# Kernel tuning notes

Hardware: AMD Instinct MI355X
Metric: run time of the kernel (lower is better)

The kernel has to match this reference:

```python
import jax, jax.numpy as jnp
import numpy as np

NH = 12  # num_heads


def setup_inputs() -> dict:
    key = jax.random.key(0)
    k1, k2, k3 = jax.random.split(key, 3)
    B, Hs, Ws, C = 8, 56, 56, 768
    N = Hs * Ws + 1  # +1 cls token
    x = jax.random.normal(k1, (B, N, C), jnp.float32)
    W_qkv = jax.random.normal(k2, (C, 3 * C), jnp.float32) * 0.02  # qkv_bias=False
    W_proj = jax.random.normal(k3, (C, C), jnp.float32) * 0.02
    b_proj = jnp.zeros((C,), jnp.float32)
    return {"x": x, "W_qkv": W_qkv, "W_proj": W_proj, "b_proj": b_proj}


def _criss_cross(x, W_qkv, W_proj, b_proj):
    B, N, C = x.shape
    H = W = int(np.sqrt(N))  # N = H*W + 1 (cls token); int(sqrt(3137)) == 56
    hd = C // NH
    scale = hd ** -0.5
    qkv = (x @ W_qkv).reshape(B, N, 3, NH, hd).transpose(2, 0, 3, 1, 4)
    q, k, v = qkv[0], qkv[1], qkv[2]  # (B, NH, N, hd)
    q_cls, k_cls, v_cls = q[:, :, :1], k[:, :, :1], v[:, :, :1]  # (B, NH, 1, hd)

    def grid(t):  # drop cls, view as spatial grid (B, NH, H, W, hd)
        return t[:, :, 1:].reshape(B, NH, H, W, hd)

    def col_view(t, t_cls):  # column (height) axis with cls prepended: (B, W, NH, 1+H, hd)
        tg = jnp.transpose(grid(t), (0, 3, 1, 2, 4))
        cls = jnp.broadcast_to(t_cls[:, None], (B, W, NH, 1, hd))
        return jnp.concatenate([cls, tg], axis=3)

    def row_view(t):  # row (width) axis: (B, H, NH, W, hd)
        return jnp.transpose(grid(t), (0, 2, 1, 3, 4))

    q_h, k_h, v_h = col_view(q, q_cls), col_view(k, k_cls), col_view(v, v_cls)
    q_w, k_w, v_w = row_view(q), row_view(k), row_view(v)

    s_h = jnp.einsum('bwnqd,bwnkd->bwnqk', q_h, k_h) * scale  # (B, W, NH, 1+H, 1+H)
    s_h = jnp.transpose(s_h, (0, 3, 2, 1, 4))[:, 1:]          # (B, H, NH, W, 1+H)
    s_w = jnp.einsum('bhnqd,bhnkd->bhnqk', q_w, k_w) * scale  # (B, H, NH, W, W)
    s_w = jnp.where(jnp.eye(W, dtype=bool), -jnp.inf, s_w)    # mask self in row attention

    # joint softmax over concatenated column+row scores
    attn = jax.nn.softmax(jnp.concatenate([s_h, s_w], axis=-1), axis=-1)
    a_h, a_w = attn[..., :1 + H], attn[..., 1 + H:]
    a_h = jnp.transpose(a_h, (0, 3, 2, 1, 4))  # (B, W, NH, H, 1+H)

    x_h = jnp.einsum('bwnqk,bwnkd->bqwnd', a_h, v_h).reshape(B, H, W, C)
    x_w = jnp.einsum('bhnqk,bhnkd->bhqnd', a_w, v_w).reshape(B, H, W, C)
    out = (x_h + x_w).reshape(B, H * W, C)

    # cls token attends over the full sequence (including itself)
    s_cls = jnp.einsum('bnqd,bnkd->bnqk', q_cls, k) * scale  # (B, NH, 1, N)
    a_cls = jax.nn.softmax(s_cls, axis=-1)
    x_cls = jnp.einsum('bnqk,bnkd->bqnd', a_cls, v).reshape(B, 1, C)

    out = jnp.concatenate([x_cls, out], axis=1)  # (B, N, C)
    return out @ W_proj + b_proj


def reference(x, W_qkv, W_proj, b_proj):
    return _criss_cross(x, W_qkv, W_proj, b_proj)
```

## Files before the change

### kernel.cpp

```cpp
#include <hip/hip_runtime.h>
#include <math.h>

#define B_   8
#define Hs   56
#define Ws   56
#define Cc   768
#define NHh  12
#define HDd  64
#define Nt   3137
#define HW_  3136
#define C3   2304
#define SCALE 0.125f
#define Mrows (B_ * Nt)
#define Mpad  (99 * 256)

typedef _Float16 half8  __attribute__((ext_vector_type(8)));
typedef _Float16 half4  __attribute__((ext_vector_type(4)));
typedef _Float16 half2_ __attribute__((ext_vector_type(2)));
typedef float floatx4 __attribute__((ext_vector_type(4)));

#define WAITV(N) asm volatile("s_waitcnt vmcnt(" #N ")" ::: "memory")
#define WAITL    asm volatile("s_waitcnt lgkmcnt(0)" ::: "memory")

__device__ __forceinline__ void barrier_mem() {
    asm volatile("" ::: "memory");
    __builtin_amdgcn_s_barrier();
    asm volatile("" ::: "memory");
}

__device__ __forceinline__ void gload_lds16(const _Float16* g, _Float16* l) {
    __builtin_amdgcn_global_load_lds(
        (const __attribute__((address_space(1))) void*)g,
        (__attribute__((address_space(3))) void*)l, 16, 0, 0);
}

__device__ _Float16 g_qkvh[(size_t)Mrows * C3];
__device__ float    g_Ocol[(size_t)B_ * NHh * HW_ * HDd];
__device__ float    g_mcol[(size_t)B_ * NHh * HW_];
__device__ float    g_lcol[(size_t)B_ * NHh * HW_];
__device__ _Float16 g_xh[(size_t)Mpad * Cc];
__device__ _Float16 g_attH[(size_t)Mpad * Cc];
__device__ _Float16 g_WqkvT[(size_t)C3 * Cc];
__device__ _Float16 g_WprojT[(size_t)Cc * Cc];
__device__ float    g_clsP[(size_t)B_ * NHh * 4 * 66];

__global__ __launch_bounds__(256) void cvt_f16(
    const float* __restrict__ in, _Float16* __restrict__ out, int n4)
{
    for (int i = blockIdx.x * 256 + threadIdx.x; i < n4; i += gridDim.x * 256) {
        float4 v = ((const float4*)in)[i];
        half4 h = { (_Float16)v.x, (_Float16)v.y, (_Float16)v.z, (_Float16)v.w };
        ((half4*)out)[i] = h;
    }
}

__global__ __launch_bounds__(256) void transpose_f16(
    const float* __restrict__ in, _Float16* __restrict__ out, int R, int Cq)
{
    __shared__ float t[32][33];
    const int c0 = blockIdx.x * 32, r0 = blockIdx.y * 32;
    const int tx = threadIdx.x & 31, ty = threadIdx.x >> 5;
#pragma unroll
    for (int i = 0; i < 32; i += 8)
        t[ty + i][tx] = in[(size_t)(r0 + ty + i) * Cq + c0 + tx];
    __syncthreads();
#pragma unroll
    for (int i = 0; i < 32; i += 8)
        out[(size_t)(c0 + ty + i) * R + r0 + tx] = (_Float16)t[tx][ty + i];
}

template <typename OutT, int BM>
__global__ __launch_bounds__(512, 2) void gemm_f16(
    const _Float16* __restrict__ A, const _Float16* __restrict__ Bt,
    const float* __restrict__ bias, OutT* __restrict__ Cm,
    int M, int Nd, int K)
{
    constexpr int MI   = BM / 32;
    constexpr int MIH  = MI / 2;
    constexpr int LA   = BM / 128;
    constexpr int ASZh = BM * 64;
    constexpr int BSZh = 256 * 64;
    constexpr size_t MAINB = (size_t)2 * (ASZh + BSZh) * 2;
    constexpr size_t EPIB  = sizeof(OutT) == 2 ? (size_t)BM * 280 * 2
                                               : (size_t)BM * 140 * 4;
    constexpr size_t SMEMB = MAINB > EPIB ? MAINB : EPIB;
    __shared__ __align__(16) char smem[SMEMB];

    const int tid = threadIdx.x;
    const int wave = tid >> 6, lane = tid & 63;
    const int wm = wave & 1, wn = wave >> 1;

    const int bid = blockIdx.y * gridDim.x + blockIdx.x;
    const int perPanel = gridDim.x * 16;
    const int panel = bid / perPanel;
    const int rowsIn = min(16, (int)gridDim.y - panel * 16);
    const int rem = bid - panel * perPanel;
    const int by = panel * 16 + rem % rowsIn;
    const int bx = rem / rowsIn;
    const int mBase = by * BM, nBase = bx * 256;

    const int rU  = ((tid >> 7) << 4) + (tid & 15);
    const int kcU = (tid >> 4) & 7;

    auto stageHalf = [&](int kt, int h) {
        _Float16* arena = (_Float16*)smem + (size_t)(kt & 1) * (ASZh + BSZh);
        if (h < 2) {
            _Float16* ldsA = arena + h * (ASZh / 2) + tid * 8;
            const _Float16* g = A + (size_t)(mBase + h * (BM / 2) + rU) * K
                                  + kt * 64 + kcU * 8;
#pragma unroll
            for (int j = 0; j < LA; ++j)
                gload_lds16(g + (size_t)j * 64 * K, ldsA + j * 4096);
        } else {
            const int hh = h - 2;
            _Float16* ldsB = arena + ASZh + hh * (BSZh / 2) + tid * 8;
            const _Float16* g = Bt + (size_t)(nBase + hh * 128 + rU) * K
                                   + kt * 64 + kcU * 8;
#pragma unroll
            for (int j = 0; j < 2; ++j)
                gload_lds16(g + (size_t)j * 64 * K, ldsB + j * 4096);
        }
    };

    const int fo = (lane >> 4) * 128 + (lane & 15) * 8;

    floatx4 acc[MI][4] = {};
    half8 a[MIH], b[4];

    const int NT = K >> 6;
    stageHalf(0, 0); stageHalf(0, 1); stageHalf(0, 2); stageHalf(0, 3);

    for (int t = 0; t < NT; ++t) {
        const _Float16* aA = (const _Float16*)smem
                             + (size_t)(t & 1) * (ASZh + BSZh);
        const _Float16* aB = aA + ASZh;
        const bool st = (t + 1 < NT);

        if (st) stageHalf(t + 1, 0);
        if (!st) { WAITV(0); }
        else if constexpr (LA == 2) { WAITV(2); }
        else { WAITV(1); }
        barrier_mem();
#pragma unroll
        for (int ni = 0; ni < 4; ++ni)
            b[ni] = *(const half8*)&aB[(wn * 4 + ni) * 1024 + fo];
#pragma unroll
        for (int mi = 0; mi < MIH; ++mi)
            a[mi] = *(const half8*)&aA[(wm * MI + mi) * 1024 + fo];
        WAITL;
        __builtin_amdgcn_s_setprio(1);
#pragma unroll
        for (int mi = 0; mi < MIH; ++mi)
#pragma unroll
            for (int ni = 0; ni < 4; ++ni)
                acc[mi][ni] = __builtin_amdgcn_mfma_f32_16x16x32_f16(
                    b[ni], a[mi], acc[mi][ni], 0, 0, 0);
        __builtin_amdgcn_s_setprio(0);
        barrier_mem();

        if (st) stageHalf(t + 1, 1);
#pragma unroll
        for (int mi = 0; mi < MIH; ++mi)
            a[mi] = *(const half8*)&aA[(wm * MI + MIH + mi) * 1024 + fo];
        WAITL;
        __builtin_amdgcn_s_setprio(1);
#pragma unroll
        for (int mi = 0; mi < MIH; ++mi)
#pragma unroll
            for (int ni = 0; ni < 4; ++ni)
                acc[MIH + mi][ni] = __builtin_amdgcn_mfma_f32_16x16x32_f16(
                    b[ni], a[mi], acc[MIH + mi][ni], 0, 0, 0);
        __builtin_amdgcn_s_setprio(0);
        barrier_mem();

        if (st) stageHalf(t + 1, 2);
#pragma unroll
        for (int ni = 0; ni < 4; ++ni)
            b[ni] = *(const half8*)&aB[(wn * 4 + ni) * 1024 + 512 + fo];
#pragma unroll
        for (int mi = 0; mi < MIH; ++mi)
            a[mi] = *(const half8*)&aA[(wm * MI + mi) * 1024 + 512 + fo];
        WAITL;
        __builtin_amdgcn_s_setprio(1);
#pragma unroll
        for (int mi = 0; mi < MIH; ++mi)
#pragma unroll
            for (int ni = 0; ni < 4; ++ni)
                acc[mi][ni] = __builtin_amdgcn_mfma_f32_16x16x32_f16(
                    b[ni], a[mi], acc[mi][ni], 0, 0, 0);
        __builtin_amdgcn_s_setprio(0);
        barrier_mem();

        if (st) stageHalf(t + 1, 3);
#pragma unroll
        for (int mi = 0; mi < MIH; ++mi)
            a[mi] = *(const half8*)&aA[(wm * MI + MIH + mi) * 1024 + 512 + fo];
        WAITL;
        __builtin_amdgcn_s_setprio(1);
#pragma unroll
        for (int mi = 0; mi < MIH; ++mi)
#pragma unroll
            for (int ni = 0; ni < 4; ++ni)
                acc[MIH + mi][ni] = __builtin_amdgcn_mfma_f32_16x16x32_f16(
                    b[ni], a[mi], acc[MIH + mi][ni], 0, 0, 0);
        __builtin_amdgcn_s_setprio(0);
        barrier_mem();
    }

    const int mlBase = wm * (BM / 2) + (lane & 15);
    const int nlBase = wn * 64 + ((lane >> 4) << 2);

    if constexpr (sizeof(OutT) == 2) {
        _Float16* Ch = (_Float16*)smem;
#pragma unroll
        for (int ni = 0; ni < 4; ++ni) {
            const int nl = nlBase + ni * 16;
#pragma unroll
            for (int mi = 0; mi < MI; ++mi) {
                const int ml = mlBase + mi * 16;
                floatx4 v = acc[mi][ni];
                half4 h = { (_Float16)v[0], (_Float16)v[1],
                            (_Float16)v[2], (_Float16)v[3] };
                *(half4*)&Ch[ml * 280 + nl] = h;
            }
        }
        barrier_mem();
#pragma unroll
        for (int i = 0; i < BM / 16; ++i) {
            const int f = i * 512 + tid;
            const int row = f >> 5, u = f & 31;
            const int gm = mBase + row;
            if (gm < M)
                *(half8*)&Cm[(size_t)gm * Nd + nBase + u * 8] =
                    *(const half8*)&Ch[row * 280 + u * 8];
        }
    } else {
        float* Cf = (float*)smem;
#pragma unroll
        for (int nh = 0; nh < 2; ++nh) {
            barrier_mem();
            if ((wn >> 1) == nh) {
#pragma unroll
                for (int ni = 0; ni < 4; ++ni) {
                    const int n0 = nBase + wn * 64 + ((lane >> 4) << 2) + ni * 16;
                    float4 bv = bias ? *(const float4*)&bias[n0]
                                     : make_float4(0.f, 0.f, 0.f, 0.f);
                    const int nl = (wn & 1) * 64 + ((lane >> 4) << 2) + ni * 16;
#pragma unroll
                    for (int mi = 0; mi < MI; ++mi) {
                        const int ml = mlBase + mi * 16;
                        floatx4 v = acc[mi][ni];
                        float4 o = make_float4(v[0] + bv.x, v[1] + bv.y,
                                               v[2] + bv.z, v[3] + bv.w);
                        *(float4*)&Cf[ml * 140 + nl] = o;
                    }
                }
            }
            barrier_mem();
#pragma unroll
            for (int i = 0; i < BM / 16; ++i) {
                const int f = i * 512 + tid;
                const int row = f >> 5, u = f & 31;
                const int gm = mBase + row;
                if (gm < M)
                    *(float4*)&Cm[(size_t)gm * Nd + nBase + nh * 128 + u * 4] =
                        *(const float4*)&Cf[row * 140 + u * 4];
            }
        }
    }
}

template <int MODE>
__global__ __launch_bounds__(64) void cc_attn(
    const _Float16* __restrict__ qkvh,
    float* __restrict__ Ocol, float* __restrict__ mcol,
    float* __restrict__ lcol, _Float16* __restrict__ attH)
{
    constexpr int NK = (MODE == 0) ? 57 : 56;
    const int x = blockIdx.x, nh = blockIdx.y, b = blockIdx.z;
    const int lane = threadIdx.x;
    const int q15 = lane & 15, g = lane >> 4;

    __shared__ __align__(16) char smem[18944];
    _Float16* Vt = (_Float16*)smem;
    _Float16* Pl = (_Float16*)(smem + 9216);
    float*    ML = (float*)(smem + 18432);
    float*    Ol = (float*)smem;

    const _Float16* base_b = qkvh + (size_t)(b * Nt) * C3 + nh * HDd;

    auto nrow_k = [&](int key) -> int {
        key = min(key, NK - 1);
        if (MODE == 0) return (key == 0) ? 0 : ((key - 1) * Ws + x + 1);
        return x * Ws + key + 1;
    };
    auto nrow_q = [&](int q) -> int {
        q = min(q, 55);
        return (MODE == 0) ? (q * Ws + x + 1) : (x * Ws + q + 1);
    };

    half8 Kf[4][2], Qf[4][2];
#pragma unroll
    for (int t = 0; t < 4; ++t) {
        const _Float16* kp = base_b + (size_t)nrow_k(t * 16 + q15) * C3 + Cc;
        const _Float16* qp = base_b + (size_t)nrow_q(t * 16 + q15) * C3;
#pragma unroll
        for (int kk = 0; kk < 2; ++kk) {
            Kf[t][kk] = *(const half8*)(kp + kk * 32 + g * 8);
            Qf[t][kk] = *(const half8*)(qp + kk * 32 + g * 8);
        }
    }

#pragma unroll
    for (int it = 0; it < 8; ++it) {
        const int i = it * 64 + lane;
        const int j = i >> 3, c = i & 7;
        half8 v = {};
        if (j < NK)
            v = *(const half8*)(base_b + (size_t)nrow_k(j) * C3 + 2 * Cc + c * 8);
#pragma unroll
        for (int e = 0; e < 8; ++e)
            Vt[(c * 8 + e) * 72 + ((j + 8 * c) & 63)] = v[e];
    }

    floatx4 S[4][4] = {};
#pragma unroll
    for (int kt = 0; kt < 4; ++kt)
#pragma unroll
        for (int qt = 0; qt < 4; ++qt)
#pragma unroll
            for (int kk = 0; kk < 2; ++kk)
                S[kt][qt] = __builtin_amdgcn_mfma_f32_16x16x32_f16(
                    Kf[kt][kk], Qf[qt][kk], S[kt][qt], 0, 0, 0);

    float mq[4], lq[4];
#pragma unroll
    for (int qt = 0; qt < 4; ++qt) {
        const int q = qt * 16 + q15;
        float sv[4][4];
        float mm = -1e30f;
#pragma unroll
        for (int kt = 0; kt < 4; ++kt)
#pragma unroll
            for (int r = 0; r < 4; ++r) {
                const int key = kt * 16 + g * 4 + r;
                float s = S[kt][qt][r] * SCALE;
                const bool bad = (key >= NK) || (MODE == 1 && key == q);
                sv[kt][r] = bad ? -1e30f : s;
                mm = fmaxf(mm, sv[kt][r]);
            }
        mm = fmaxf(mm, __shfl_xor(mm, 16, 64));
        mm = fmaxf(mm, __shfl_xor(mm, 32, 64));
        float ll = 0.f;
#pragma unroll
        for (int kt = 0; kt < 4; ++kt) {
            half4 ph;
#pragma unroll
            for (int r = 0; r < 4; ++r) {
                const float p = __expf(sv[kt][r] - mm);
                ll += p;
                ph[r] = (_Float16)p;
            }
            *(half4*)&Pl[q * 72 + kt * 16 + g * 4] = ph;
        }
        ll += __shfl_xor(ll, 16, 64);
        ll += __shfl_xor(ll, 32, 64);
        mq[qt] = mm; lq[qt] = ll;
    }

    if (g == 0) {
        if (MODE == 0) {
#pragma unroll
            for (int qt = 0; qt < 4; ++qt) {
                const int q = qt * 16 + q15;
                if (q < 56) {
                    const size_t qi = (size_t)((b * NHh + nh) * HW_) + q * Ws + x;
                    mcol[qi] = mq[qt]; lcol[qi] = lq[qt];
                }
            }
        } else {
#pragma unroll
            for (int qt = 0; qt < 4; ++qt) {
                ML[qt * 16 + q15] = mq[qt];
                ML[64 + qt * 16 + q15] = lq[qt];
            }
        }
    }
    __syncthreads();

    half8 Pf[4][2];
#pragma unroll
    for (int qt = 0; qt < 4; ++qt)
#pragma unroll
        for (int kk = 0; kk < 2; ++kk)
            Pf[qt][kk] = *(const half8*)&Pl[(qt * 16 + q15) * 72 + kk * 32 + g * 8];

    floatx4 O[4][4] = {};
#pragma unroll
    for (int dt = 0; dt < 4; ++dt) {
        const int d = dt * 16 + q15;
        const int rot = 8 * (d >> 3);
        half8 Vf0 = *(const half8*)&Vt[d * 72 + ((0 + g * 8 + rot) & 63)];
        half8 Vf1 = *(const half8*)&Vt[d * 72 + ((32 + g * 8 + rot) & 63)];
#pragma unroll
        for (int qt = 0; qt < 4; ++qt) {
            O[dt][qt] = __builtin_amdgcn_mfma_f32_16x16x32_f16(
                Vf0, Pf[qt][0], O[dt][qt], 0, 0, 0);
            O[dt][qt] = __builtin_amdgcn_mfma_f32_16x16x32_f16(
                Vf1, Pf[qt][1], O[dt][qt], 0, 0, 0);
        }
    }
    __syncthreads();

#pragma unroll
    for (int dt = 0; dt < 4; ++dt)
#pragma unroll
        for (int qt = 0; qt < 4; ++qt) {
            float4 f = { O[dt][qt][0], O[dt][qt][1], O[dt][qt][2], O[dt][qt][3] };
            *(float4*)&Ol[(qt * 16 + q15) * 68 + dt * 16 + g * 4] = f;
        }
    __syncthreads();

    const int qq = lane;
    if (qq < 56) {
        if (MODE == 0) {
            const size_t qi = (size_t)((b * NHh + nh) * HW_) + qq * Ws + x;
            float* op = Ocol + qi * HDd;
#pragma unroll
            for (int i = 0; i < 16; ++i)
                *(float4*)(op + i * 4) = *(const float4*)&Ol[qq * 68 + i * 4];
        } else {
            const size_t qi = (size_t)((b * NHh + nh) * HW_) + x * Ws + qq;
            const float mc = mcol[qi], lc = lcol[qi];
            const float mr = ML[qq], lr = ML[64 + qq];
            const float mn = fmaxf(mc, mr);
            const float fc = __expf(mc - mn);
            const float fr = __expf(mr - mn);
            const float inv = 1.f / (lc * fc + lr * fr);
            const int n = x * Ws + qq + 1;
            _Float16* op = attH + (size_t)(b * Nt + n) * Cc + nh * HDd;
            const float* ocp = Ocol + qi * HDd;
#pragma unroll
            for (int i = 0; i < 16; ++i) {
                float4 oc = *(const float4*)(ocp + i * 4);
                const float* oo = &Ol[qq * 68 + i * 4];
                half4 r = { (_Float16)((oc.x * fc + oo[0] * fr) * inv),
                            (_Float16)((oc.y * fc + oo[1] * fr) * inv),
                            (_Float16)((oc.z * fc + oo[2] * fr) * inv),
                            (_Float16)((oc.w * fc + oo[3] * fr) * inv) };
                *(half4*)(op + i * 4) = r;
            }
        }
    }
}

__global__ __launch_bounds__(1024) void cls_part(
    const _Float16* __restrict__ qkvh, float* __restrict__ P)
{
    const int nh = blockIdx.x, b = blockIdx.y, sidx = blockIdx.z;
    const int j0 = sidx * 785, j1 = min(Nt, j0 + 785);
    const int tid = threadIdx.x;
    const int lane = tid & 63, wv = tid >> 6;

    const float qd = (float)qkvh[(size_t)(b * Nt) * C3 + nh * HDd + lane];
    float m = -INFINITY, l = 0.f, Od = 0.f;

    for (int j = j0 + wv; j < j1; j += 16) {
        const _Float16* base = qkvh + (size_t)(b * Nt + j) * C3 + nh * HDd;
        float prod = qd * (float)base[Cc + lane];
#pragma unroll
        for (int off = 32; off >= 1; off >>= 1)
            prod += __shfl_xor(prod, off, 64);
        float s = prod * SCALE;
        float mn = fmaxf(m, s);
        float corr = __expf(m - mn);
        float p = __expf(s - mn);
        l = l * corr + p;
        Od = fmaf(Od, corr, p * (float)base[2 * Cc + lane]);
        m = mn;
    }

    __shared__ float sm[16], sl[16], sO[16][64];
    if (lane == 0) { sm[wv] = m; sl[wv] = l; }
    sO[wv][lane] = Od;
    __syncthreads();

    if (tid < 64) {
        float M2 = sm[0];
#pragma unroll
        for (int i = 1; i < 16; ++i) M2 = fmaxf(M2, sm[i]);
        float L = 0.f, OO = 0.f;
#pragma unroll
        for (int i = 0; i < 16; ++i) {
            float f = __expf(sm[i] - M2);
            L += sl[i] * f;
            OO += sO[i][tid] * f;
        }
        float* pp = P + (size_t)((b * NHh + nh) * 4 + sidx) * 66;
        if (tid == 0) { pp[0] = M2; pp[1] = L; }
        pp[2 + tid] = OO;
    }
}

__global__ __launch_bounds__(64) void cls_merge(
    const float* __restrict__ P, _Float16* __restrict__ attH)
{
    const int nh = blockIdx.x, b = blockIdx.y;
    const int tid = threadIdx.x;
    const float* p0 = P + (size_t)(b * NHh + nh) * 4 * 66;
    float M2 = fmaxf(fmaxf(p0[0], p0[66]), fmaxf(p0[132], p0[198]));
    float L = 0.f, OO = 0.f;
#pragma unroll
    for (int i = 0; i < 4; ++i) {
        const float* pp = p0 + i * 66;
        float f = __expf(pp[0] - M2);
        L += pp[1] * f;
        OO += pp[2 + tid] * f;
    }
    attH[(size_t)(b * Nt) * Cc + nh * HDd + tid] = (_Float16)(OO / L);
}

extern "C" void kernel_launch(void* const* d_in, const int* in_sizes, int n_in,
                              void* d_out, int out_size, void* d_ws, size_t ws_size,
                              hipStream_t stream)
{
    const float* x     = (const float*)d_in[0];
    const float* Wqkv  = (const float*)d_in[1];
    const float* Wproj = (const float*)d_in[2];
    const float* bproj = (const float*)d_in[3];
    float* out = (float*)d_out;

    _Float16* qkvh;   hipGetSymbolAddress((void**)&qkvh,   HIP_SYMBOL(g_qkvh));
    float*    Ocol;   hipGetSymbolAddress((void**)&Ocol,   HIP_SYMBOL(g_Ocol));
    float*    mcol;   hipGetSymbolAddress((void**)&mcol,   HIP_SYMBOL(g_mcol));
    float*    lcol;   hipGetSymbolAddress((void**)&lcol,   HIP_SYMBOL(g_lcol));
    _Float16* xh;     hipGetSymbolAddress((void**)&xh,     HIP_SYMBOL(g_xh));
    _Float16* attH;   hipGetSymbolAddress((void**)&attH,   HIP_SYMBOL(g_attH));
    _Float16* WqkvT;  hipGetSymbolAddress((void**)&WqkvT,  HIP_SYMBOL(g_WqkvT));
    _Float16* WprojT; hipGetSymbolAddress((void**)&WprojT, HIP_SYMBOL(g_WprojT));
    float*    clsP;   hipGetSymbolAddress((void**)&clsP,   HIP_SYMBOL(g_clsP));

    cvt_f16<<<4096, 256, 0, stream>>>(x, xh, (Mrows * Cc) / 4);
    transpose_f16<<<dim3(C3 / 32, Cc / 32), 256, 0, stream>>>(Wqkv, WqkvT, Cc, C3);
    transpose_f16<<<dim3(Cc / 32, Cc / 32), 256, 0, stream>>>(Wproj, WprojT, Cc, Cc);

    gemm_f16<_Float16, 256><<<dim3(C3 / 256, Mpad / 256), 512, 0, stream>>>(
        xh, WqkvT, nullptr, qkvh, Mrows, C3, Cc);

    cc_attn<0><<<dim3(Ws, NHh, B_), 64, 0, stream>>>(qkvh, Ocol, mcol, lcol, attH);
    cls_part<<<dim3(NHh, B_, 4), 1024, 0, stream>>>(qkvh, clsP);
    cls_merge<<<dim3(NHh, B_), 64, 0, stream>>>(clsP, attH);
    cc_attn<1><<<dim3(Hs, NHh, B_), 64, 0, stream>>>(qkvh, Ocol, mcol, lcol, attH);

    gemm_f16<float, 128><<<dim3(Cc / 256, Mpad / 128), 512, 0, stream>>>(
        attH, WprojT, bproj, out, Mrows, Cc, Cc);
}
```

Measured before the change: 504.0 us.

## Restructure GEMM main loop into 4-stage K=32 pipeline with register double-buffering

Replaces the double-buffered K=64 tile loop, which used four barrier-separated sub-phases, with a four-slot ring of K=32 tiles staged three ahead, and one barrier per tile. LDS fragments for the next tile are read into a second register set while the current tile's MFMAs run, so LDS latency hides behind compute. This adds fragment registers, which pressures occupancy at launch bounds (512,2). The tighter vmcnt accounting also risks hazards, and the NT loop steps by two, which assumes an even tile count.

```diff
diff --git a/kernel.cpp b/kernel.cpp
--- a/kernel.cpp
+++ b/kernel.cpp
@@ -76,11 +76,11 @@
     int M, int Nd, int K)
 {
     constexpr int MI   = BM / 32;
-    constexpr int MIH  = MI / 2;
     constexpr int LA   = BM / 128;
-    constexpr int ASZh = BM * 64;
-    constexpr int BSZh = 256 * 64;
-    constexpr size_t MAINB = (size_t)2 * (ASZh + BSZh) * 2;
+    constexpr int ASZh = BM * 32;
+    constexpr int BSZh = 256 * 32;
+    constexpr int BUFh = ASZh + BSZh;
+    constexpr size_t MAINB = (size_t)4 * BUFh * 2;
     constexpr size_t EPIB  = sizeof(OutT) == 2 ? (size_t)BM * 280 * 2
                                                : (size_t)BM * 140 * 4;
     constexpr size_t SMEMB = MAINB > EPIB ? MAINB : EPIB;
@@ -99,113 +99,72 @@
     const int bx = rem / rowsIn;
     const int mBase = by * BM, nBase = bx * 256;
 
-    const int rU  = ((tid >> 7) << 4) + (tid & 15);
-    const int kcU = (tid >> 4) & 7;
-
-    auto stageHalf = [&](int kt, int h) {
-        _Float16* arena = (_Float16*)smem + (size_t)(kt & 1) * (ASZh + BSZh);
-        if (h < 2) {
-            _Float16* ldsA = arena + h * (ASZh / 2) + tid * 8;
-            const _Float16* g = A + (size_t)(mBase + h * (BM / 2) + rU) * K
-                                  + kt * 64 + kcU * 8;
-#pragma unroll
-            for (int j = 0; j < LA; ++j)
-                gload_lds16(g + (size_t)j * 64 * K, ldsA + j * 4096);
+    const int mU  = ((tid >> 6) << 4) + (tid & 15);
+    const int kcU = (tid >> 4) & 3;
+    const _Float16* ga = A  + (size_t)(mBase + mU) * K + kcU * 8;
+    const _Float16* gb = Bt + (size_t)(nBase + mU) * K + kcU * 8;
+
+    auto stage = [&](int t) {
+        char* base = smem + (size_t)(t & 3) * (BUFh * 2);
+        _Float16* lA = (_Float16*)base + wave * 512;
+        _Float16* lB = (_Float16*)base + ASZh + wave * 512;
+        const _Float16* gaK = ga + t * 32;
+        const _Float16* gbK = gb + t * 32;
+#pragma unroll
+        for (int i = 0; i < LA; ++i)
+            gload_lds16(gaK + (size_t)i * 128 * K, lA + i * 4096);
+#pragma unroll
+        for (int i = 0; i < 2; ++i)
+            gload_lds16(gbK + (size_t)i * 128 * K, lB + i * 4096);
+    };
+
+    const int fo = (lane >> 4) * 128 + (lane & 15) * 8;
+    auto readFrags = [&](int t, half8 (&a)[MI], half8 (&b)[4]) {
+        const _Float16* bufA = (const _Float16*)(smem + (size_t)(t & 3) * (BUFh * 2));
+        const _Float16* bufB = bufA + ASZh;
+#pragma unroll
+        for (int mi = 0; mi < MI; ++mi)
+            a[mi] = *(const half8*)&bufA[(wm * MI + mi) * 512 + fo];
+#pragma unroll
+        for (int ni = 0; ni < 4; ++ni)
+            b[ni] = *(const half8*)&bufB[(wn * 4 + ni) * 512 + fo];
+    };
+
+    floatx4 acc[MI][4] = {};
+    half8 aX[MI], bX[4], aY[MI], bY[4];
+
+    const int NT = K >> 5;
+    stage(0); stage(1); stage(2);
+    if constexpr (LA == 2) { WAITV(8); } else { WAITV(6); }
+    barrier_mem();
+    readFrags(0, aX, bX);
+
+    auto tileBody = [&](int t, half8 (&aC)[MI], half8 (&bC)[4],
+                        half8 (&aN)[MI], half8 (&bN)[4]) {
+        if (t <= NT - 3) {
+            if constexpr (LA == 2) { WAITV(4); } else { WAITV(3); }
         } else {
-            const int hh = h - 2;
-            _Float16* ldsB = arena + ASZh + hh * (BSZh / 2) + tid * 8;
-            const _Float16* g = Bt + (size_t)(nBase + hh * 128 + rU) * K
-                                   + kt * 64 + kcU * 8;
-#pragma unroll
-            for (int j = 0; j < 2; ++j)
-                gload_lds16(g + (size_t)j * 64 * K, ldsB + j * 4096);
-        }
-    };
-
-    const int fo = (lane >> 4) * 128 + (lane & 15) * 8;
-
-    floatx4 acc[MI][4] = {};
-    half8 a[MIH], b[4];
-
-    const int NT = K >> 6;
-    stageHalf(0, 0); stageHalf(0, 1); stageHalf(0, 2); stageHalf(0, 3);
-
-    for (int t = 0; t < NT; ++t) {
-        const _Float16* aA = (const _Float16*)smem
-                             + (size_t)(t & 1) * (ASZh + BSZh);
-        const _Float16* aB = aA + ASZh;
-        const bool st = (t + 1 < NT);
-
-        if (st) stageHalf(t + 1, 0);
-        if (!st) { WAITV(0); }
-        else if constexpr (LA == 2) { WAITV(2); }
-        else { WAITV(1); }
+            WAITV(0);
+        }
         barrier_mem();
-#pragma unroll
-        for (int ni = 0; ni < 4; ++ni)
-            b[ni] = *(const half8*)&aB[(wn * 4 + ni) * 1024 + fo];
-#pragma unroll
-        for (int mi = 0; mi < MIH; ++mi)
-            a[mi] = *(const half8*)&aA[(wm * MI + mi) * 1024 + fo];
-        WAITL;
+        if (t + 3 < NT) stage(t + 3);
         __builtin_amdgcn_s_setprio(1);
-#pragma unroll
-        for (int mi = 0; mi < MIH; ++mi)
+        if (t + 1 < NT) readFrags(t + 1, aN, bN);
+#pragma unroll
+        for (int mi = 0; mi < MI; ++mi)
 #pragma unroll
             for (int ni = 0; ni < 4; ++ni)
                 acc[mi][ni] = __builtin_amdgcn_mfma_f32_16x16x32_f16(
-                    b[ni], a[mi], acc[mi][ni], 0, 0, 0);
+                    bC[ni], aC[mi], acc[mi][ni], 0, 0, 0);
         __builtin_amdgcn_s_setprio(0);
-        barrier_mem();
-
-        if (st) stageHalf(t + 1, 1);
-#pragma unroll
-        for (int mi = 0; mi < MIH; ++mi)
-            a[mi] = *(const half8*)&aA[(wm * MI + MIH + mi) * 1024 + fo];
-        WAITL;
-        __builtin_amdgcn_s_setprio(1);
-#pragma unroll
-        for (int mi = 0; mi < MIH; ++mi)
-#pragma unroll
-            for (int ni = 0; ni < 4; ++ni)
-                acc[MIH + mi][ni] = __builtin_amdgcn_mfma_f32_16x16x32_f16(
-                    b[ni], a[mi], acc[MIH + mi][ni], 0, 0, 0);
-        __builtin_amdgcn_s_setprio(0);
-        barrier_mem();
-
-        if (st) stageHalf(t + 1, 2);
-#pragma unroll
-        for (int ni = 0; ni < 4; ++ni)
-            b[ni] = *(const half8*)&aB[(wn * 4 + ni) * 1024 + 512 + fo];
-#pragma unroll
-        for (int mi = 0; mi < MIH; ++mi)
-            a[mi] = *(const half8*)&aA[(wm * MI + mi) * 1024 + 512 + fo];
-        WAITL;
-        __builtin_amdgcn_s_setprio(1);
-#pragma unroll
-        for (int mi = 0; mi < MIH; ++mi)
-#pragma unroll
-            for (int ni = 0; ni < 4; ++ni)
-                acc[mi][ni] = __builtin_amdgcn_mfma_f32_16x16x32_f16(
-                    b[ni], a[mi], acc[mi][ni], 0, 0, 0);
-        __builtin_amdgcn_s_setprio(0);
-        barrier_mem();
-
-        if (st) stageHalf(t + 1, 3);
-#pragma unroll
-        for (int mi = 0; mi < MIH; ++mi)
-            a[mi] = *(const half8*)&aA[(wm * MI + MIH + mi) * 1024 + 512 + fo];
-        WAITL;
-        __builtin_amdgcn_s_setprio(1);
-#pragma unroll
-        for (int mi = 0; mi < MIH; ++mi)
-#pragma unroll
-            for (int ni = 0; ni < 4; ++ni)
-                acc[MIH + mi][ni] = __builtin_amdgcn_mfma_f32_16x16x32_f16(
-                    b[ni], a[mi], acc[MIH + mi][ni], 0, 0, 0);
-        __builtin_amdgcn_s_setprio(0);
-        barrier_mem();
-    }
+    };
+
+    for (int t = 0; t < NT; t += 2) {
+        tileBody(t,     aX, bX, aY, bY);
+        tileBody(t + 1, aY, bY, aX, bX);
+    }
+    WAITL;
+    barrier_mem();
 
     const int mlBase = wm * (BM / 2) + (lane & 15);
     const int nlBase = wn * 64 + ((lane >> 4) << 2);
```

Result: faster. 482.7 us (-4.2%).
